# Kernel tuning notes

Hardware: AMD Instinct MI355X
Metric: run time of the kernel (lower is better)

## Reference

```python
import jax, jax.numpy as jnp
import numpy as np

HID = 512
HEADS = 8
HD = HID // HEADS
PF = 2048
EPS = 1e-5


def _layer_norm(x, g, b):
    m = jnp.mean(x, axis=-1, keepdims=True)
    v = jnp.mean((x - m) ** 2, axis=-1, keepdims=True)
    return (x - m) * jax.lax.rsqrt(v + EPS) * g + b


def setup_inputs() -> dict:
    key = jax.random.key(0)
    ks = jax.random.split(key, 24)
    s = 0.02
    p = {}
    p["src"] = jax.random.normal(ks[0], (2, 512, HID), dtype=jnp.float32)
    p["src_mask"] = jnp.ones((2, 1, 1, 512), dtype=jnp.int32)
    # projection weights stored as (in, out); Linear math y = x @ W + b
    p["Wq"] = jax.random.normal(ks[1], (HID, HID), dtype=jnp.float32) * s
    p["bq"] = jnp.zeros((HID,), jnp.float32)
    p["Wk"] = jax.random.normal(ks[2], (HID, HID), dtype=jnp.float32) * s
    p["bk"] = jnp.zeros((HID,), jnp.float32)
    p["Wv"] = jax.random.normal(ks[3], (HID, HID), dtype=jnp.float32) * s
    p["bv"] = jnp.zeros((HID,), jnp.float32)
    p["Wo"] = jax.random.normal(ks[4], (HID, HID), dtype=jnp.float32) * s
    p["bo"] = jnp.zeros((HID,), jnp.float32)
    # additive-attention params (per-head_dim)
    p["Wa"] = jax.random.normal(ks[5], (HD, HD), dtype=jnp.float32) * s
    p["ba"] = jnp.zeros((HD,), jnp.float32)
    p["Ua"] = jax.random.normal(ks[6], (HD, HD), dtype=jnp.float32) * s
    p["ub"] = jnp.zeros((HD,), jnp.float32)
    p["Vw"] = jax.random.normal(ks[7], (HD,), dtype=jnp.float32) * s
    p["Vb"] = jnp.zeros((), jnp.float32)
    # layer norms
    p["ln1_g"] = jnp.ones((HID,), jnp.float32)
    p["ln1_b"] = jnp.zeros((HID,), jnp.float32)
    p["ln2_g"] = jnp.ones((HID,), jnp.float32)
    p["ln2_b"] = jnp.zeros((HID,), jnp.float32)
    # FFN
    p["W1"] = jax.random.normal(ks[8], (HID, PF), dtype=jnp.float32) * s
    p["b1"] = jnp.zeros((PF,), jnp.float32)
    p["W2"] = jax.random.normal(ks[9], (PF, HID), dtype=jnp.float32) * s
    p["b2"] = jnp.zeros((HID,), jnp.float32)
    return p


def reference(src, src_mask, Wq, bq, Wk, bk, Wv, bv, Wo, bo,
              Wa, ba, Ua, ub, Vw, Vb, ln1_g, ln1_b, ln2_g, ln2_b,
              W1, b1, W2, b2):
    B, L, D = src.shape
    # project and split heads: (B, H, L, hd)
    def heads(x):
        return x.reshape(B, L, HEADS, HD).transpose(0, 2, 1, 3)
    Q = heads(src @ Wq + bq)
    K = heads(src @ Wk + bk)
    V = heads(src @ Wv + bv)
    Qa = Q @ Wa + ba          # (B,H,L,hd)
    Ka = K @ Ua + ub          # (B,H,L,hd)
    # additive (Bahdanau) scores: tanh broadcast to (B,H,Lq,Lk,hd), reduce with Vw
    t = jnp.tanh(Qa[:, :, :, None, :] + Ka[:, :, None, :, :])
    energy = jnp.einsum('bhqkd,d->bhqk', t, Vw) + Vb
    energy = jnp.where(src_mask == 0, jnp.float32(-1e10), energy)
    attention = jax.nn.softmax(energy, axis=-1)
    x = jnp.einsum('bhqk,bhkd->bhqd', attention, V)
    x = x.transpose(0, 2, 1, 3).reshape(B, L, D)
    attn_out = x @ Wo + bo
    src1 = _layer_norm(src + attn_out, ln1_g, ln1_b)
    ffn = jax.nn.relu(src1 @ W1 + b1) @ W2 + b2
    return _layer_norm(src1 + ffn, ln2_g, ln2_b)
```

## Files before the change

### kernel.cpp

```cpp
#include <hip/hip_runtime.h>

#define HID 512
#define HEADS 8
#define HD 64
#define PF 2048
#define LEN 512
#define EPS 1e-5f
#define LOG2E 1.44269504f

typedef __bf16 bf16x8 __attribute__((ext_vector_type(8)));
typedef float  f32x4  __attribute__((ext_vector_type(4)));

#define TC0 0.99990220f
#define TC1 (-0.33032631f)
#define TC2 0.11820859f
#define TC3 (-0.02619031f)
#define G3C1  (-0.99097893f)
#define G5C2  (0.59104295f)
#define G7C3  (-0.18333217f)
#define G10C2 (1.18208590f)
#define G21C3 (-0.54999651f)
#define G35C3 (-0.91666085f)

__device__ __forceinline__ void fuse_body(
    const float* __restrict__ Wbig, const float* __restrict__ Wsm,
    const float* __restrict__ bbig, const float* __restrict__ bsm,
    __bf16* __restrict__ outT, float* __restrict__ bout,
    int cchunk, int h, int t, float* smem) {
    float* wb_s = smem;
    float* wsm_s = smem + 4096;
    const int c0 = cchunk * 64;
    const int col = t & 63, rq = t >> 6;
    #pragma unroll
    for (int i = 0; i < 16; ++i) {
        int r = rq * 16 + i;
        wb_s[r * 64 + col]  = Wbig[(size_t)(c0 + r) * HID + h * 64 + col];
        wsm_s[r * 64 + col] = Wsm[r * 64 + col];
    }
    __syncthreads();
    float acc[16] = {};
    for (int d = 0; d < 64; ++d) {
        float wl = wsm_s[d * 64 + col];
        #pragma unroll
        for (int i = 0; i < 16; ++i)
            acc[i] += wb_s[(rq * 16 + i) * 64 + d] * wl;
    }
    #pragma unroll
    for (int i = 0; i < 16; ++i)
        outT[(size_t)(h * 64 + col) * HID + c0 + rq * 16 + i] = (__bf16)acc[i];
    if (cchunk == 0 && t < 64) {
        float bacc = bsm[col];
        for (int d = 0; d < 64; ++d)
            bacc += bbig[h * 64 + d] * wsm_s[d * 64 + col];
        bout[h * 64 + col] = bacc;
    }
}

__device__ __forceinline__ void cast_t_body(
    const float* __restrict__ W, __bf16* __restrict__ WT,
    int K, int N, int n0, int k0, int t, float* smem) {
    float* tile = smem;
    const int tx = t & 31, ty = t >> 5;
    #pragma unroll
    for (int i = 0; i < 4; ++i)
        tile[(ty + 8 * i) * 33 + tx] = W[(size_t)(k0 + ty + 8 * i) * N + n0 + tx];
    __syncthreads();
    #pragma unroll
    for (int i = 0; i < 4; ++i)
        WT[(size_t)(n0 + ty + 8 * i) * K + k0 + tx] = (__bf16)tile[tx * 33 + ty + 8 * i];
}

__global__ __launch_bounds__(256) void prep_all(
    const float* __restrict__ Wq, const float* __restrict__ Wa,
    const float* __restrict__ bq, const float* __restrict__ ba,
    const float* __restrict__ Wk, const float* __restrict__ Ua,
    const float* __restrict__ bk, const float* __restrict__ ub,
    const float* __restrict__ Wv, const float* __restrict__ bv,
    const float* __restrict__ Wo, const float* __restrict__ W1,
    const float* __restrict__ W2, const float* __restrict__ src,
    __bf16* __restrict__ WqkvT, float* __restrict__ bqkv,
    __bf16* __restrict__ WoT, __bf16* __restrict__ W1T,
    __bf16* __restrict__ W2T, __bf16* __restrict__ src_bf) {
    __shared__ float smem[8192];
    const int bid = blockIdx.x;
    const int t = threadIdx.x;
    if (bid < 64) {
        fuse_body(Wq, Wa, bq, ba, WqkvT, bqkv, bid & 7, bid >> 3, t, smem);
    } else if (bid < 128) {
        int q = bid - 64;
        fuse_body(Wk, Ua, bk, ub, WqkvT + (size_t)512 * HID, bqkv + 512, q & 7, q >> 3, t, smem);
    } else if (bid < 384) {
        int q = bid - 128;
        cast_t_body(Wv, WqkvT + (size_t)1024 * HID, HID, HID, (q & 15) * 32, (q >> 4) * 32, t, smem);
    } else if (bid < 640) {
        int q = bid - 384;
        cast_t_body(Wo, WoT, HID, HID, (q & 15) * 32, (q >> 4) * 32, t, smem);
    } else if (bid < 1664) {
        int q = bid - 640;
        cast_t_body(W1, W1T, HID, PF, (q & 63) * 32, (q >> 6) * 32, t, smem);
    } else if (bid < 2688) {
        int q = bid - 1664;
        cast_t_body(W2, W2T, PF, HID, (q & 15) * 32, (q >> 4) * 32, t, smem);
    } else if (bid < 2690) {
        int q = bid - 2688;
        bqkv[1024 + q * 256 + t] = bv[q * 256 + t];
    } else {
        int q = bid - 2690;
        int i = q * 256 + t;
        src_bf[i] = (__bf16)src[i];
    }
}

template <bool RELU, bool OUT_BF16, int KS>
__global__ __launch_bounds__(64) void gemm_mfma(
    const __bf16* __restrict__ A, const __bf16* __restrict__ BT,
    const float* __restrict__ bias, float* __restrict__ Cf,
    __bf16* __restrict__ Cb, int M, int N, int K) {
    const int m0 = blockIdx.x * 64;
    const int n0 = blockIdx.y * 64;
    const int ks = (KS > 1) ? blockIdx.z : 0;
    const int Kc = K / KS;
    const int l = threadIdx.x;
    const int r16 = l & 15;
    const int kof = (l >> 4) * 8 + ks * Kc;

    f32x4 acc[4][4] = {};
    const __bf16* Ap = A + (size_t)(m0 + r16) * K + kof;
    const __bf16* Bp = BT + (size_t)(n0 + r16) * K + kof;

    #pragma unroll 4
    for (int k0 = 0; k0 < Kc; k0 += 32) {
        bf16x8 a[4], b[4];
        #pragma unroll
        for (int mr = 0; mr < 4; ++mr)
            a[mr] = *(const bf16x8*)(Ap + (size_t)mr * 16 * K + k0);
        #pragma unroll
        for (int nr = 0; nr < 4; ++nr)
            b[nr] = *(const bf16x8*)(Bp + (size_t)nr * 16 * K + k0);
        #pragma unroll
        for (int mr = 0; mr < 4; ++mr)
            #pragma unroll
            for (int nr = 0; nr < 4; ++nr)
                acc[mr][nr] = __builtin_amdgcn_mfma_f32_16x16x32_bf16(a[mr], b[nr], acc[mr][nr], 0, 0, 0);
    }

    const int crow = (l >> 4) * 4;
    const int ccol = l & 15;
    float* Co = Cf + (size_t)ks * M * N;
    #pragma unroll
    for (int mr = 0; mr < 4; ++mr) {
        #pragma unroll
        for (int nr = 0; nr < 4; ++nr) {
            int n = n0 + nr * 16 + ccol;
            float bs = (ks == 0) ? bias[n] : 0.f;
            #pragma unroll
            for (int r = 0; r < 4; ++r) {
                int m = m0 + mr * 16 + crow + r;
                float v = acc[mr][nr][r] + bs;
                if (RELU) v = fmaxf(v, 0.f);
                if (OUT_BF16) Cb[(size_t)m * N + n] = (__bf16)v;
                else          Co[(size_t)m * N + n] = v;
            }
        }
    }
}

__global__ __launch_bounds__(64) void qkv_feat(
    const __bf16* __restrict__ A, const __bf16* __restrict__ BT,
    const float* __restrict__ bqkv, const float* __restrict__ Vw,
    __bf16* __restrict__ Af, __bf16* __restrict__ Bf,
    __bf16* __restrict__ VT) {
    __shared__ float tile[64][65];
    const int m0 = blockIdx.x * 64;
    const int by = blockIdx.y;
    const int n0 = by * 64;
    const int type = by >> 3;
    const int h = by & 7;
    const int b = m0 >> 9;
    const int bh = b * 8 + h;
    const int l0 = m0 & 511;
    const int l = threadIdx.x;
    const int r16 = l & 15;
    const int g = l >> 4;
    const int kof = g * 8;

    f32x4 acc[4][4] = {};
    const __bf16* Ap = A + (size_t)(m0 + r16) * HID + kof;
    const __bf16* Bp = BT + (size_t)(n0 + r16) * HID + kof;
    #pragma unroll 4
    for (int k0 = 0; k0 < HID; k0 += 32) {
        bf16x8 a[4], bb[4];
        #pragma unroll
        for (int mr = 0; mr < 4; ++mr)
            a[mr] = *(const bf16x8*)(Ap + (size_t)mr * 16 * HID + k0);
        #pragma unroll
        for (int nr = 0; nr < 4; ++nr)
            bb[nr] = *(const bf16x8*)(Bp + (size_t)nr * 16 * HID + k0);
        #pragma unroll
        for (int mr = 0; mr < 4; ++mr)
            #pragma unroll
            for (int nr = 0; nr < 4; ++nr)
                acc[mr][nr] = __builtin_amdgcn_mfma_f32_16x16x32_bf16(a[mr], bb[nr], acc[mr][nr], 0, 0, 0);
    }

    const int crow = g * 4;
    const int ccol = r16;
    if (type == 0) {
        #pragma unroll
        for (int nr = 0; nr < 4; ++nr) {
            int d = nr * 16 + ccol;
            float bs = bqkv[n0 + d];
            #pragma unroll
            for (int mr = 0; mr < 4; ++mr)
                #pragma unroll
                for (int r = 0; r < 4; ++r) {
                    int lrow = l0 + mr * 16 + crow + r;
                    float x = acc[mr][nr][r] + bs;
                    float x2 = x * x, x3 = x2 * x, x4 = x2 * x2, x6 = x4 * x2;
                    bf16x8 f;
                    f[0] = (__bf16)1.0f; f[1] = (__bf16)x;
                    f[2] = (__bf16)x2;   f[3] = (__bf16)x3;
                    f[4] = (__bf16)x4;   f[5] = (__bf16)(x4 * x);
                    f[6] = (__bf16)x6;   f[7] = (__bf16)(x6 * x);
                    *(bf16x8*)(Af + ((size_t)(bh * LEN + lrow)) * 512 + d * 8) = f;
                }
        }
    } else if (type == 1) {
        #pragma unroll
        for (int nr = 0; nr < 4; ++nr) {
            int d = nr * 16 + ccol;
            float bs = bqkv[n0 + d];
            float w = Vw[d];
            #pragma unroll
            for (int mr = 0; mr < 4; ++mr)
                #pragma unroll
                for (int r = 0; r < 4; ++r) {
                    int lrow = l0 + mr * 16 + crow + r;
                    float y = acc[mr][nr][r] + bs;
                    float y2 = y * y;
                    bf16x8 f;
                    f[0] = (__bf16)(w * (y * (((TC3 * y2 + TC2) * y2 + TC1) * y2 + TC0)));
                    f[1] = (__bf16)(w * (((G7C3 * y2 + G5C2) * y2 + G3C1) * y2 + TC0));
                    f[2] = (__bf16)(w * (y * ((G21C3 * y2 + G10C2) * y2 + G3C1)));
                    f[3] = (__bf16)(w * ((G35C3 * y2 + G10C2) * y2 + TC1));
                    f[4] = (__bf16)(w * (y * (G35C3 * y2 + G5C2)));
                    f[5] = (__bf16)(w * (G21C3 * y2 + TC2));
                    f[6] = (__bf16)(w * (G7C3 * y));
                    f[7] = (__bf16)(w * TC3);
                    *(bf16x8*)(Bf + ((size_t)(bh * LEN + lrow)) * 512 + d * 8) = f;
                }
        }
    } else {
        #pragma unroll
        for (int nr = 0; nr < 4; ++nr) {
            int d = nr * 16 + ccol;
            float bs = bqkv[n0 + d];
            #pragma unroll
            for (int mr = 0; mr < 4; ++mr)
                #pragma unroll
                for (int r = 0; r < 4; ++r)
                    tile[mr * 16 + crow + r][d] = acc[mr][nr][r] + bs;
        }
        __syncthreads();
        for (int dd = 0; dd < 64; ++dd)
            VT[((size_t)(bh * 64 + dd)) * LEN + l0 + l] = (__bf16)tile[l][dd];
    }
}

__global__ __launch_bounds__(256) void attn_psum(
    const __bf16* __restrict__ Af, const __bf16* __restrict__ Bf,
    const __bf16* __restrict__ VT, const int* __restrict__ mask,
    __bf16* __restrict__ X) {
    __shared__ __align__(16) char pls[32 * 1024];
    __shared__ float psum[4][16][64];
    __shared__ float rs[32][5];
    const int bid = blockIdx.x;
    const int wgid = (bid & 7) * 32 + (bid >> 3);
    const int bh = wgid >> 4;
    const int m0 = (wgid & 15) * 32;
    const int b = bh >> 3, h = bh & 7;
    const int w = threadIdx.x >> 6;
    const int l = threadIdx.x & 63;
    const int r16 = l & 15, g = l >> 4, kof = g * 8;
    const int c0 = w * 128;

    const __bf16* Ap = Af + ((size_t)(bh * LEN + m0 + r16)) * 512 + kof;
    const __bf16* Bp = Bf + ((size_t)(bh * LEN + c0 + r16)) * 512 + kof;

    f32x4 acc[2][8] = {};
    #pragma unroll 4
    for (int k0 = 0; k0 < 512; k0 += 32) {
        bf16x8 a0 = *(const bf16x8*)(Ap + k0);
        bf16x8 a1 = *(const bf16x8*)(Ap + 16 * 512 + k0);
        #pragma unroll
        for (int nr = 0; nr < 8; ++nr) {
            bf16x8 bb = *(const bf16x8*)(Bp + (size_t)nr * 16 * 512 + k0);
            acc[0][nr] = __builtin_amdgcn_mfma_f32_16x16x32_bf16(a0, bb, acc[0][nr], 0, 0, 0);
            acc[1][nr] = __builtin_amdgcn_mfma_f32_16x16x32_bf16(a1, bb, acc[1][nr], 0, 0, 0);
        }
    }

    float rsum[2][4] = {};
    #pragma unroll
    for (int nr = 0; nr < 8; ++nr) {
        int col = c0 + nr * 16 + r16;
        float mk = (mask[b * LEN + col] == 0) ? 0.f : 1.f;
        #pragma unroll
        for (int mr = 0; mr < 2; ++mr)
            #pragma unroll
            for (int r = 0; r < 4; ++r) {
                float pv = __builtin_amdgcn_exp2f(acc[mr][nr][r] * LOG2E) * mk;
                acc[mr][nr][r] = pv;
                rsum[mr][r] += pv;
            }
    }
    #pragma unroll
    for (int off = 1; off <= 8; off <<= 1)
        #pragma unroll
        for (int mr = 0; mr < 2; ++mr)
            #pragma unroll
            for (int r = 0; r < 4; ++r)
                rsum[mr][r] += __shfl_xor(rsum[mr][r], off);
    if (r16 == 0) {
        #pragma unroll
        for (int mr = 0; mr < 2; ++mr)
            #pragma unroll
            for (int r = 0; r < 4; ++r)
                rs[mr * 16 + g * 4 + r][w] = rsum[mr][r];
    }
    __syncthreads();
    float inv_[2][4];
    #pragma unroll
    for (int mr = 0; mr < 2; ++mr)
        #pragma unroll
        for (int r = 0; r < 4; ++r) {
            int row = mr * 16 + g * 4 + r;
            float tot = rs[row][0] + rs[row][1] + rs[row][2] + rs[row][3];
            inv_[mr][r] = __builtin_amdgcn_rcpf(tot);
        }
    #pragma unroll
    for (int mr = 0; mr < 2; ++mr)
        #pragma unroll
        for (int nr = 0; nr < 8; ++nr) {
            int col = c0 + nr * 16 + r16;
            #pragma unroll
            for (int r = 0; r < 4; ++r) {
                int row = mr * 16 + g * 4 + r;
                int byte = (row * 1024 + col * 2) ^ ((row & 7) << 4);
                *(__bf16*)(pls + byte) = (__bf16)(acc[mr][nr][r] * inv_[mr][r]);
            }
        }
    __syncthreads();

    const int rh = w >> 1, kh = w & 1;
    f32x4 oc[4] = {};
    const __bf16* Vp = VT + ((size_t)(bh * 64 + r16)) * LEN + kh * 256 + kof;
    #pragma unroll 4
    for (int k0 = 0; k0 < 256; k0 += 32) {
        int row = rh * 16 + r16;
        int byte = (row * 1024 + (kh * 256 + k0 + kof) * 2) ^ ((row & 7) << 4);
        bf16x8 pa = *(const bf16x8*)(pls + byte);
        #pragma unroll
        for (int nr = 0; nr < 4; ++nr) {
            bf16x8 vb = *(const bf16x8*)(Vp + (size_t)nr * 16 * LEN + k0);
            oc[nr] = __builtin_amdgcn_mfma_f32_16x16x32_bf16(pa, vb, oc[nr], 0, 0, 0);
        }
    }
    #pragma unroll
    for (int nr = 0; nr < 4; ++nr)
        #pragma unroll
        for (int r = 0; r < 4; ++r)
            psum[w][g * 4 + r][nr * 16 + r16] = oc[nr][r];
    __syncthreads();
    for (int i = threadIdx.x; i < 32 * 64; i += 256) {
        int row = i >> 6, d = i & 63;
        int rh2 = row >> 4, rr = row & 15;
        float v = psum[rh2 * 2][rr][d] + psum[rh2 * 2 + 1][rr][d];
        X[(size_t)(b * LEN + m0 + row) * HID + h * 64 + d] = (__bf16)v;
    }
}

template <bool WB, int NS>
__global__ __launch_bounds__(256) void ln_kernel(
    const float* __restrict__ A, const float* __restrict__ Bsrc,
    const float* __restrict__ g, const float* __restrict__ beta,
    float* __restrict__ out, __bf16* __restrict__ outb) {
    const int row = blockIdx.x;
    const int t = threadIdx.x;
    float x0 = Bsrc[(size_t)row * HID + t];
    float x1 = Bsrc[(size_t)row * HID + t + 256];
    #pragma unroll
    for (int s = 0; s < NS; ++s) {
        x0 += A[(size_t)s * 524288 + (size_t)row * HID + t];
        x1 += A[(size_t)s * 524288 + (size_t)row * HID + t + 256];
    }
    float s0 = x0 + x1, ss = x0 * x0 + x1 * x1;
    #pragma unroll
    for (int off = 32; off; off >>= 1) {
        s0 += __shfl_xor(s0, off);
        ss += __shfl_xor(ss, off);
    }
    __shared__ float rsm[4], rss[4];
    const int lane = t & 63, wv = t >> 6;
    if (lane == 0) { rsm[wv] = s0; rss[wv] = ss; }
    __syncthreads();
    s0 = rsm[0] + rsm[1] + rsm[2] + rsm[3];
    ss = rss[0] + rss[1] + rss[2] + rss[3];
    float mean = s0 * (1.0f / HID);
    float var = ss * (1.0f / HID) - mean * mean;
    float inv = rsqrtf(var + EPS);
    float y0 = (x0 - mean) * inv * g[t] + beta[t];
    float y1 = (x1 - mean) * inv * g[t + 256] + beta[t + 256];
    out[(size_t)row * HID + t] = y0;
    out[(size_t)row * HID + t + 256] = y1;
    if (WB) {
        outb[(size_t)row * HID + t] = (__bf16)y0;
        outb[(size_t)row * HID + t + 256] = (__bf16)y1;
    }
}


extern "C" void kernel_launch(void* const* d_in, const int* in_sizes, int n_in,
                              void* d_out, int out_size, void* d_ws, size_t ws_size,
                              hipStream_t stream) {
    const float* src   = (const float*)d_in[0];
    const int*   mask  = (const int*)d_in[1];
    const float* Wq    = (const float*)d_in[2];
    const float* bq    = (const float*)d_in[3];
    const float* Wk    = (const float*)d_in[4];
    const float* bk    = (const float*)d_in[5];
    const float* Wv    = (const float*)d_in[6];
    const float* bv    = (const float*)d_in[7];
    const float* Wo    = (const float*)d_in[8];
    const float* bo    = (const float*)d_in[9];
    const float* Wa    = (const float*)d_in[10];
    const float* ba    = (const float*)d_in[11];
    const float* Ua    = (const float*)d_in[12];
    const float* ub    = (const float*)d_in[13];
    const float* Vw    = (const float*)d_in[14];
    const float* ln1g  = (const float*)d_in[16];
    const float* ln1b  = (const float*)d_in[17];
    const float* ln2g  = (const float*)d_in[18];
    const float* ln2b  = (const float*)d_in[19];
    const float* W1    = (const float*)d_in[20];
    const float* b1    = (const float*)d_in[21];
    const float* W2    = (const float*)d_in[22];
    const float* b2    = (const float*)d_in[23];
    float* out = (float*)d_out;

    float* ws = (float*)d_ws;
    size_t off = 0;
    auto alloc = [&](size_t nf) { float* p = ws + off; off += nf; return p; };

    __bf16* WqkvT  = (__bf16*)alloc(393216);
    __bf16* WoT    = (__bf16*)alloc(131072);
    __bf16* W1T    = (__bf16*)alloc(524288);
    __bf16* W2T    = (__bf16*)alloc(524288);
    float*  bqkv   = alloc(1536);
    __bf16* src_bf = (__bf16*)alloc(262144);
    __bf16* Af     = (__bf16*)alloc(2097152);
    __bf16* Bf     = (__bf16*)alloc(2097152);
    __bf16* VT     = (__bf16*)alloc(262144);
    __bf16* x_bf   = (__bf16*)alloc(262144);
    float*  tmp    = alloc(2097152);
    float*  src1   = alloc(524288);
    __bf16* s1_bf  = (__bf16*)alloc(262144);
    __bf16* h1     = (__bf16*)alloc(1048576);

    const int M = 2 * LEN;

    prep_all<<<4738, 256, 0, stream>>>(Wq, Wa, bq, ba, Wk, Ua, bk, ub,
                                       Wv, bv, Wo, W1, W2, src,
                                       WqkvT, bqkv, WoT, W1T, W2T, src_bf);

    qkv_feat<<<dim3(16, 24), 64, 0, stream>>>(src_bf, WqkvT, bqkv, Vw, Af, Bf, VT);

    attn_psum<<<256, 256, 0, stream>>>(Af, Bf, VT, mask, x_bf);

    gemm_mfma<false, false, 2><<<dim3(16, 8, 2), 64, 0, stream>>>(
        x_bf, WoT, bo, tmp, nullptr, M, HID, HID);

    ln_kernel<true, 2><<<M, 256, 0, stream>>>(tmp, src, ln1g, ln1b, src1, s1_bf);

    gemm_mfma<true, true, 1><<<dim3(16, 32), 64, 0, stream>>>(
        s1_bf, W1T, b1, nullptr, h1, M, PF, HID);

    gemm_mfma<false, false, 4><<<dim3(16, 8, 4), 64, 0, stream>>>(
        h1, W2T, b2, tmp, nullptr, M, HID, PF);

    ln_kernel<false, 4><<<M, 256, 0, stream>>>(tmp, src1, ln2g, ln2b, out, nullptr);
}
```

Baseline: 102.2 us.

## Fuse all stages into one cooperative persistent kernel with grid syncs

Replaces the eight separate kernel launches with a single cooperative kernel of 256 blocks. Grid-wide barriers separate the stages, and each stage distributes its work units over blocks or waves. The goal is to remove launch gaps and per-kernel ramp-up between the short stages. The V transpose becomes its own stage through a raw buffer, and layer norm is rewritten to handle one row per wave with vector loads. The costs are grid.sync overhead, lower occupancy from a large shared-memory footprint, and fixed parallelism of 256 blocks.

New measurement: 385.1 us. +276.9%, slower.

```diff
diff --git a/kernel.cpp b/kernel.cpp
--- a/kernel.cpp
+++ b/kernel.cpp
@@ -1,4 +1,7 @@
 #include <hip/hip_runtime.h>
+#include <hip/hip_cooperative_groups.h>
+
+namespace cg = cooperative_groups;
 
 #define HID 512
 #define HEADS 8
@@ -22,6 +25,19 @@
 #define G21C3 (-0.54999651f)
 #define G35C3 (-0.91666085f)
 
+struct MegaArgs {
+    const float* src; const int* mask;
+    const float *Wq, *bq, *Wk, *bk, *Wv, *bv, *Wo, *bo;
+    const float *Wa, *ba, *Ua, *ub, *Vw;
+    const float *ln1g, *ln1b, *ln2g, *ln2b;
+    const float *W1, *b1, *W2, *b2;
+    float* out;
+    __bf16* WqkvT; float* bqkv;
+    __bf16 *WoT, *W1T, *W2T, *src_bf, *Af, *Bf, *vraw, *VT, *x_bf;
+    float *tmp, *src1;
+    __bf16 *s1_bf, *h1;
+};
+
 __device__ __forceinline__ void fuse_body(
     const float* __restrict__ Wbig, const float* __restrict__ Wsm,
     const float* __restrict__ bbig, const float* __restrict__ bsm,
@@ -70,57 +86,15 @@
         WT[(size_t)(n0 + ty + 8 * i) * K + k0 + tx] = (__bf16)tile[tx * 33 + ty + 8 * i];
 }
 
-__global__ __launch_bounds__(256) void prep_all(
-    const float* __restrict__ Wq, const float* __restrict__ Wa,
-    const float* __restrict__ bq, const float* __restrict__ ba,
-    const float* __restrict__ Wk, const float* __restrict__ Ua,
-    const float* __restrict__ bk, const float* __restrict__ ub,
-    const float* __restrict__ Wv, const float* __restrict__ bv,
-    const float* __restrict__ Wo, const float* __restrict__ W1,
-    const float* __restrict__ W2, const float* __restrict__ src,
-    __bf16* __restrict__ WqkvT, float* __restrict__ bqkv,
-    __bf16* __restrict__ WoT, __bf16* __restrict__ W1T,
-    __bf16* __restrict__ W2T, __bf16* __restrict__ src_bf) {
-    __shared__ float smem[8192];
-    const int bid = blockIdx.x;
-    const int t = threadIdx.x;
-    if (bid < 64) {
-        fuse_body(Wq, Wa, bq, ba, WqkvT, bqkv, bid & 7, bid >> 3, t, smem);
-    } else if (bid < 128) {
-        int q = bid - 64;
-        fuse_body(Wk, Ua, bk, ub, WqkvT + (size_t)512 * HID, bqkv + 512, q & 7, q >> 3, t, smem);
-    } else if (bid < 384) {
-        int q = bid - 128;
-        cast_t_body(Wv, WqkvT + (size_t)1024 * HID, HID, HID, (q & 15) * 32, (q >> 4) * 32, t, smem);
-    } else if (bid < 640) {
-        int q = bid - 384;
-        cast_t_body(Wo, WoT, HID, HID, (q & 15) * 32, (q >> 4) * 32, t, smem);
-    } else if (bid < 1664) {
-        int q = bid - 640;
-        cast_t_body(W1, W1T, HID, PF, (q & 63) * 32, (q >> 6) * 32, t, smem);
-    } else if (bid < 2688) {
-        int q = bid - 1664;
-        cast_t_body(W2, W2T, PF, HID, (q & 15) * 32, (q >> 4) * 32, t, smem);
-    } else if (bid < 2690) {
-        int q = bid - 2688;
-        bqkv[1024 + q * 256 + t] = bv[q * 256 + t];
-    } else {
-        int q = bid - 2690;
-        int i = q * 256 + t;
-        src_bf[i] = (__bf16)src[i];
-    }
-}
-
 template <bool RELU, bool OUT_BF16, int KS>
-__global__ __launch_bounds__(64) void gemm_mfma(
+__device__ __forceinline__ void gemm_wave(
     const __bf16* __restrict__ A, const __bf16* __restrict__ BT,
     const float* __restrict__ bias, float* __restrict__ Cf,
-    __bf16* __restrict__ Cb, int M, int N, int K) {
-    const int m0 = blockIdx.x * 64;
-    const int n0 = blockIdx.y * 64;
-    const int ks = (KS > 1) ? blockIdx.z : 0;
+    __bf16* __restrict__ Cb, int M, int N, int K,
+    int bx, int by, int ks, int l) {
+    const int m0 = bx * 64;
+    const int n0 = by * 64;
     const int Kc = K / KS;
-    const int l = threadIdx.x;
     const int r16 = l & 15;
     const int kof = (l >> 4) * 8 + ks * Kc;
 
@@ -165,34 +139,28 @@
     }
 }
 
-__global__ __launch_bounds__(64) void qkv_feat(
-    const __bf16* __restrict__ A, const __bf16* __restrict__ BT,
-    const float* __restrict__ bqkv, const float* __restrict__ Vw,
-    __bf16* __restrict__ Af, __bf16* __restrict__ Bf,
-    __bf16* __restrict__ VT) {
-    __shared__ float tile[64][65];
-    const int m0 = blockIdx.x * 64;
-    const int by = blockIdx.y;
+__device__ __forceinline__ void qkv_wave(const MegaArgs& a, int u, int l) {
+    const int bx = u & 15, by = u >> 4;
+    const int m0 = bx * 64;
     const int n0 = by * 64;
     const int type = by >> 3;
     const int h = by & 7;
     const int b = m0 >> 9;
     const int bh = b * 8 + h;
     const int l0 = m0 & 511;
-    const int l = threadIdx.x;
     const int r16 = l & 15;
     const int g = l >> 4;
     const int kof = g * 8;
 
     f32x4 acc[4][4] = {};
-    const __bf16* Ap = A + (size_t)(m0 + r16) * HID + kof;
-    const __bf16* Bp = BT + (size_t)(n0 + r16) * HID + kof;
+    const __bf16* Ap = a.src_bf + (size_t)(m0 + r16) * HID + kof;
+    const __bf16* Bp = a.WqkvT + (size_t)(n0 + r16) * HID + kof;
     #pragma unroll 4
     for (int k0 = 0; k0 < HID; k0 += 32) {
-        bf16x8 a[4], bb[4];
+        bf16x8 av[4], bb[4];
         #pragma unroll
         for (int mr = 0; mr < 4; ++mr)
-            a[mr] = *(const bf16x8*)(Ap + (size_t)mr * 16 * HID + k0);
+            av[mr] = *(const bf16x8*)(Ap + (size_t)mr * 16 * HID + k0);
         #pragma unroll
         for (int nr = 0; nr < 4; ++nr)
             bb[nr] = *(const bf16x8*)(Bp + (size_t)nr * 16 * HID + k0);
@@ -200,16 +168,15 @@
         for (int mr = 0; mr < 4; ++mr)
             #pragma unroll
             for (int nr = 0; nr < 4; ++nr)
-                acc[mr][nr] = __builtin_amdgcn_mfma_f32_16x16x32_bf16(a[mr], bb[nr], acc[mr][nr], 0, 0, 0);
+                acc[mr][nr] = __builtin_amdgcn_mfma_f32_16x16x32_bf16(av[mr], bb[nr], acc[mr][nr], 0, 0, 0);
     }
 
     const int crow = g * 4;
-    const int ccol = r16;
     if (type == 0) {
         #pragma unroll
         for (int nr = 0; nr < 4; ++nr) {
-            int d = nr * 16 + ccol;
-            float bs = bqkv[n0 + d];
+            int d = nr * 16 + r16;
+            float bs = a.bqkv[n0 + d];
             #pragma unroll
             for (int mr = 0; mr < 4; ++mr)
                 #pragma unroll
@@ -222,15 +189,15 @@
                     f[2] = (__bf16)x2;   f[3] = (__bf16)x3;
                     f[4] = (__bf16)x4;   f[5] = (__bf16)(x4 * x);
                     f[6] = (__bf16)x6;   f[7] = (__bf16)(x6 * x);
-                    *(bf16x8*)(Af + ((size_t)(bh * LEN + lrow)) * 512 + d * 8) = f;
+                    *(bf16x8*)(a.Af + ((size_t)(bh * LEN + lrow)) * 512 + d * 8) = f;
                 }
         }
     } else if (type == 1) {
         #pragma unroll
         for (int nr = 0; nr < 4; ++nr) {
-            int d = nr * 16 + ccol;
-            float bs = bqkv[n0 + d];
-            float w = Vw[d];
+            int d = nr * 16 + r16;
+            float bs = a.bqkv[n0 + d];
+            float w = a.Vw[d];
             #pragma unroll
             for (int mr = 0; mr < 4; ++mr)
                 #pragma unroll
@@ -247,246 +214,309 @@
                     f[5] = (__bf16)(w * (G21C3 * y2 + TC2));
                     f[6] = (__bf16)(w * (G7C3 * y));
                     f[7] = (__bf16)(w * TC3);
-                    *(bf16x8*)(Bf + ((size_t)(bh * LEN + lrow)) * 512 + d * 8) = f;
+                    *(bf16x8*)(a.Bf + ((size_t)(bh * LEN + lrow)) * 512 + d * 8) = f;
                 }
         }
     } else {
         #pragma unroll
         for (int nr = 0; nr < 4; ++nr) {
-            int d = nr * 16 + ccol;
-            float bs = bqkv[n0 + d];
+            int d = nr * 16 + r16;
+            float bs = a.bqkv[1024 + h * 64 + d];
             #pragma unroll
             for (int mr = 0; mr < 4; ++mr)
                 #pragma unroll
-                for (int r = 0; r < 4; ++r)
-                    tile[mr * 16 + crow + r][d] = acc[mr][nr][r] + bs;
-        }
-        __syncthreads();
-        for (int dd = 0; dd < 64; ++dd)
-            VT[((size_t)(bh * 64 + dd)) * LEN + l0 + l] = (__bf16)tile[l][dd];
-    }
-}
-
-__global__ __launch_bounds__(256) void attn_psum(
-    const __bf16* __restrict__ Af, const __bf16* __restrict__ Bf,
-    const __bf16* __restrict__ VT, const int* __restrict__ mask,
-    __bf16* __restrict__ X) {
-    __shared__ __align__(16) char pls[32 * 1024];
-    __shared__ float psum[4][16][64];
-    __shared__ float rs[32][5];
-    const int bid = blockIdx.x;
-    const int wgid = (bid & 7) * 32 + (bid >> 3);
-    const int bh = wgid >> 4;
-    const int m0 = (wgid & 15) * 32;
-    const int b = bh >> 3, h = bh & 7;
-    const int w = threadIdx.x >> 6;
-    const int l = threadIdx.x & 63;
-    const int r16 = l & 15, g = l >> 4, kof = g * 8;
-    const int c0 = w * 128;
-
-    const __bf16* Ap = Af + ((size_t)(bh * LEN + m0 + r16)) * 512 + kof;
-    const __bf16* Bp = Bf + ((size_t)(bh * LEN + c0 + r16)) * 512 + kof;
-
-    f32x4 acc[2][8] = {};
-    #pragma unroll 4
-    for (int k0 = 0; k0 < 512; k0 += 32) {
-        bf16x8 a0 = *(const bf16x8*)(Ap + k0);
-        bf16x8 a1 = *(const bf16x8*)(Ap + 16 * 512 + k0);
-        #pragma unroll
-        for (int nr = 0; nr < 8; ++nr) {
-            bf16x8 bb = *(const bf16x8*)(Bp + (size_t)nr * 16 * 512 + k0);
-            acc[0][nr] = __builtin_amdgcn_mfma_f32_16x16x32_bf16(a0, bb, acc[0][nr], 0, 0, 0);
-            acc[1][nr] = __builtin_amdgcn_mfma_f32_16x16x32_bf16(a1, bb, acc[1][nr], 0, 0, 0);
-        }
-    }
-
-    float rsum[2][4] = {};
-    #pragma unroll
-    for (int nr = 0; nr < 8; ++nr) {
-        int col = c0 + nr * 16 + r16;
-        float mk = (mask[b * LEN + col] == 0) ? 0.f : 1.f;
-        #pragma unroll
-        for (int mr = 0; mr < 2; ++mr)
-            #pragma unroll
-            for (int r = 0; r < 4; ++r) {
-                float pv = __builtin_amdgcn_exp2f(acc[mr][nr][r] * LOG2E) * mk;
-                acc[mr][nr][r] = pv;
-                rsum[mr][r] += pv;
-            }
-    }
-    #pragma unroll
-    for (int off = 1; off <= 8; off <<= 1)
-        #pragma unroll
-        for (int mr = 0; mr < 2; ++mr)
-            #pragma unroll
-            for (int r = 0; r < 4; ++r)
-                rsum[mr][r] += __shfl_xor(rsum[mr][r], off);
-    if (r16 == 0) {
-        #pragma unroll
-        for (int mr = 0; mr < 2; ++mr)
-            #pragma unroll
-            for (int r = 0; r < 4; ++r)
-                rs[mr * 16 + g * 4 + r][w] = rsum[mr][r];
-    }
-    __syncthreads();
-    float inv_[2][4];
-    #pragma unroll
-    for (int mr = 0; mr < 2; ++mr)
-        #pragma unroll
-        for (int r = 0; r < 4; ++r) {
-            int row = mr * 16 + g * 4 + r;
-            float tot = rs[row][0] + rs[row][1] + rs[row][2] + rs[row][3];
-            inv_[mr][r] = __builtin_amdgcn_rcpf(tot);
-        }
-    #pragma unroll
-    for (int mr = 0; mr < 2; ++mr)
-        #pragma unroll
-        for (int nr = 0; nr < 8; ++nr) {
-            int col = c0 + nr * 16 + r16;
-            #pragma unroll
-            for (int r = 0; r < 4; ++r) {
-                int row = mr * 16 + g * 4 + r;
-                int byte = (row * 1024 + col * 2) ^ ((row & 7) << 4);
-                *(__bf16*)(pls + byte) = (__bf16)(acc[mr][nr][r] * inv_[mr][r]);
-            }
-        }
-    __syncthreads();
-
-    const int rh = w >> 1, kh = w & 1;
-    f32x4 oc[4] = {};
-    const __bf16* Vp = VT + ((size_t)(bh * 64 + r16)) * LEN + kh * 256 + kof;
-    #pragma unroll 4
-    for (int k0 = 0; k0 < 256; k0 += 32) {
-        int row = rh * 16 + r16;
-        int byte = (row * 1024 + (kh * 256 + k0 + kof) * 2) ^ ((row & 7) << 4);
-        bf16x8 pa = *(const bf16x8*)(pls + byte);
-        #pragma unroll
-        for (int nr = 0; nr < 4; ++nr) {
-            bf16x8 vb = *(const bf16x8*)(Vp + (size_t)nr * 16 * LEN + k0);
-            oc[nr] = __builtin_amdgcn_mfma_f32_16x16x32_bf16(pa, vb, oc[nr], 0, 0, 0);
-        }
-    }
-    #pragma unroll
-    for (int nr = 0; nr < 4; ++nr)
-        #pragma unroll
-        for (int r = 0; r < 4; ++r)
-            psum[w][g * 4 + r][nr * 16 + r16] = oc[nr][r];
-    __syncthreads();
-    for (int i = threadIdx.x; i < 32 * 64; i += 256) {
-        int row = i >> 6, d = i & 63;
-        int rh2 = row >> 4, rr = row & 15;
-        float v = psum[rh2 * 2][rr][d] + psum[rh2 * 2 + 1][rr][d];
-        X[(size_t)(b * LEN + m0 + row) * HID + h * 64 + d] = (__bf16)v;
+                for (int r = 0; r < 4; ++r) {
+                    int m = m0 + mr * 16 + crow + r;
+                    a.vraw[(size_t)m * 512 + h * 64 + d] = (__bf16)(acc[mr][nr][r] + bs);
+                }
+        }
     }
 }
 
 template <bool WB, int NS>
-__global__ __launch_bounds__(256) void ln_kernel(
+__device__ __forceinline__ void ln_row(
     const float* __restrict__ A, const float* __restrict__ Bsrc,
     const float* __restrict__ g, const float* __restrict__ beta,
-    float* __restrict__ out, __bf16* __restrict__ outb) {
-    const int row = blockIdx.x;
-    const int t = threadIdx.x;
-    float x0 = Bsrc[(size_t)row * HID + t];
-    float x1 = Bsrc[(size_t)row * HID + t + 256];
+    float* __restrict__ out, __bf16* __restrict__ outb, int row, int lane) {
+    const int c = lane * 8;
+    f32x4 v0 = *(const f32x4*)(Bsrc + (size_t)row * HID + c);
+    f32x4 v1 = *(const f32x4*)(Bsrc + (size_t)row * HID + c + 4);
     #pragma unroll
     for (int s = 0; s < NS; ++s) {
-        x0 += A[(size_t)s * 524288 + (size_t)row * HID + t];
-        x1 += A[(size_t)s * 524288 + (size_t)row * HID + t + 256];
-    }
-    float s0 = x0 + x1, ss = x0 * x0 + x1 * x1;
+        v0 += *(const f32x4*)(A + (size_t)s * 524288 + (size_t)row * HID + c);
+        v1 += *(const f32x4*)(A + (size_t)s * 524288 + (size_t)row * HID + c + 4);
+    }
+    float s0 = 0.f, ss = 0.f;
+    #pragma unroll
+    for (int j = 0; j < 4; ++j) { s0 += v0[j] + v1[j]; ss += v0[j] * v0[j] + v1[j] * v1[j]; }
     #pragma unroll
     for (int off = 32; off; off >>= 1) {
         s0 += __shfl_xor(s0, off);
         ss += __shfl_xor(ss, off);
     }
-    __shared__ float rsm[4], rss[4];
-    const int lane = t & 63, wv = t >> 6;
-    if (lane == 0) { rsm[wv] = s0; rss[wv] = ss; }
-    __syncthreads();
-    s0 = rsm[0] + rsm[1] + rsm[2] + rsm[3];
-    ss = rss[0] + rss[1] + rss[2] + rss[3];
     float mean = s0 * (1.0f / HID);
     float var = ss * (1.0f / HID) - mean * mean;
     float inv = rsqrtf(var + EPS);
-    float y0 = (x0 - mean) * inv * g[t] + beta[t];
-    float y1 = (x1 - mean) * inv * g[t + 256] + beta[t + 256];
-    out[(size_t)row * HID + t] = y0;
-    out[(size_t)row * HID + t + 256] = y1;
+    f32x4 g0 = *(const f32x4*)(g + c), g1 = *(const f32x4*)(g + c + 4);
+    f32x4 b0 = *(const f32x4*)(beta + c), b1 = *(const f32x4*)(beta + c + 4);
+    f32x4 y0, y1;
+    #pragma unroll
+    for (int j = 0; j < 4; ++j) {
+        y0[j] = (v0[j] - mean) * inv * g0[j] + b0[j];
+        y1[j] = (v1[j] - mean) * inv * g1[j] + b1[j];
+    }
+    *(f32x4*)(out + (size_t)row * HID + c) = y0;
+    *(f32x4*)(out + (size_t)row * HID + c + 4) = y1;
     if (WB) {
-        outb[(size_t)row * HID + t] = (__bf16)y0;
-        outb[(size_t)row * HID + t + 256] = (__bf16)y1;
-    }
+        bf16x8 yb;
+        #pragma unroll
+        for (int j = 0; j < 4; ++j) { yb[j] = (__bf16)y0[j]; yb[4 + j] = (__bf16)y1[j]; }
+        *(bf16x8*)(outb + (size_t)row * HID + c) = yb;
+    }
+}
+
+__global__ __launch_bounds__(256, 2) void mega(MegaArgs a) {
+    __shared__ __align__(16) char lds[49792];
+    cg::grid_group grid = cg::this_grid();
+    const int t = threadIdx.x;
+    const int nb = gridDim.x;
+    const int nw = nb * 4;
+    const int wid = blockIdx.x * 4 + (t >> 6);
+    const int l = t & 63;
+
+    for (int u = blockIdx.x; u < 4738; u += nb) {
+        float* smem = (float*)lds;
+        if (u < 64) {
+            fuse_body(a.Wq, a.Wa, a.bq, a.ba, a.WqkvT, a.bqkv, u & 7, u >> 3, t, smem);
+        } else if (u < 128) {
+            int q = u - 64;
+            fuse_body(a.Wk, a.Ua, a.bk, a.ub, a.WqkvT + (size_t)512 * HID, a.bqkv + 512, q & 7, q >> 3, t, smem);
+        } else if (u < 384) {
+            int q = u - 128;
+            cast_t_body(a.Wv, a.WqkvT + (size_t)1024 * HID, HID, HID, (q & 15) * 32, (q >> 4) * 32, t, smem);
+        } else if (u < 640) {
+            int q = u - 384;
+            cast_t_body(a.Wo, a.WoT, HID, HID, (q & 15) * 32, (q >> 4) * 32, t, smem);
+        } else if (u < 1664) {
+            int q = u - 640;
+            cast_t_body(a.W1, a.W1T, HID, PF, (q & 63) * 32, (q >> 6) * 32, t, smem);
+        } else if (u < 2688) {
+            int q = u - 1664;
+            cast_t_body(a.W2, a.W2T, PF, HID, (q & 15) * 32, (q >> 4) * 32, t, smem);
+        } else if (u < 2690) {
+            int q = u - 2688;
+            a.bqkv[1024 + q * 256 + t] = a.bv[q * 256 + t];
+        } else {
+            int q = u - 2690;
+            int i = q * 256 + t;
+            a.src_bf[i] = (__bf16)a.src[i];
+        }
+        __syncthreads();
+    }
+    grid.sync();
+
+    for (int u = wid; u < 384; u += nw) qkv_wave(a, u, l);
+    grid.sync();
+
+    for (int u = blockIdx.x; u < 128; u += nb) {
+        float* tile = (float*)lds;
+        const int bh = u >> 3, b = bh >> 3, h = bh & 7;
+        const int k0 = (u & 7) * 64;
+        const int tx = t & 63, ty = t >> 6;
+        #pragma unroll
+        for (int i = 0; i < 16; ++i) {
+            int r = ty + 4 * i;
+            tile[r * 65 + tx] = (float)a.vraw[(size_t)(b * LEN + k0 + r) * 512 + h * 64 + tx];
+        }
+        __syncthreads();
+        #pragma unroll
+        for (int i = 0; i < 16; ++i) {
+            int dd = ty + 4 * i;
+            a.VT[((size_t)(bh * 64 + dd)) * LEN + k0 + tx] = (__bf16)tile[tx * 65 + dd];
+        }
+        __syncthreads();
+    }
+    grid.sync();
+
+    for (int u = blockIdx.x; u < 256; u += nb) {
+        char* pls = lds;
+        float* psum = (float*)(lds + 32768);
+        float* rs = (float*)(lds + 32768 + 16384);
+        const int wgid = (u & 7) * 32 + (u >> 3);
+        const int bh = wgid >> 4;
+        const int m0 = (wgid & 15) * 32;
+        const int b = bh >> 3, h = bh & 7;
+        const int w = t >> 6;
+        const int r16 = l & 15, g = l >> 4, kof = g * 8;
+        const int c0 = w * 128;
+
+        const __bf16* Ap = a.Af + ((size_t)(bh * LEN + m0 + r16)) * 512 + kof;
+        const __bf16* Bp = a.Bf + ((size_t)(bh * LEN + c0 + r16)) * 512 + kof;
+
+        f32x4 acc[2][8] = {};
+        #pragma unroll 4
+        for (int k0 = 0; k0 < 512; k0 += 32) {
+            bf16x8 a0 = *(const bf16x8*)(Ap + k0);
+            bf16x8 a1 = *(const bf16x8*)(Ap + 16 * 512 + k0);
+            #pragma unroll
+            for (int nr = 0; nr < 8; ++nr) {
+                bf16x8 bb = *(const bf16x8*)(Bp + (size_t)nr * 16 * 512 + k0);
+                acc[0][nr] = __builtin_amdgcn_mfma_f32_16x16x32_bf16(a0, bb, acc[0][nr], 0, 0, 0);
+                acc[1][nr] = __builtin_amdgcn_mfma_f32_16x16x32_bf16(a1, bb, acc[1][nr], 0, 0, 0);
+            }
+        }
+
+        float rsum[2][4] = {};
+        #pragma unroll
+        for (int nr = 0; nr < 8; ++nr) {
+            int col = c0 + nr * 16 + r16;
+            float mk = (a.mask[b * LEN + col] == 0) ? 0.f : 1.f;
+            #pragma unroll
+            for (int mr = 0; mr < 2; ++mr)
+                #pragma unroll
+                for (int r = 0; r < 4; ++r) {
+                    float pv = __builtin_amdgcn_exp2f(acc[mr][nr][r] * LOG2E) * mk;
+                    acc[mr][nr][r] = pv;
+                    rsum[mr][r] += pv;
+                }
+        }
+        #pragma unroll
+        for (int off = 1; off <= 8; off <<= 1)
+            #pragma unroll
+            for (int mr = 0; mr < 2; ++mr)
+                #pragma unroll
+                for (int r = 0; r < 4; ++r)
+                    rsum[mr][r] += __shfl_xor(rsum[mr][r], off);
+        if (r16 == 0) {
+            #pragma unroll
+            for (int mr = 0; mr < 2; ++mr)
+                #pragma unroll
+                for (int r = 0; r < 4; ++r)
+                    rs[(mr * 16 + g * 4 + r) * 5 + w] = rsum[mr][r];
+        }
+        __syncthreads();
+        float inv_[2][4];
+        #pragma unroll
+        for (int mr = 0; mr < 2; ++mr)
+            #pragma unroll
+            for (int r = 0; r < 4; ++r) {
+                int row = mr * 16 + g * 4 + r;
+                float tot = rs[row * 5 + 0] + rs[row * 5 + 1] + rs[row * 5 + 2] + rs[row * 5 + 3];
+                inv_[mr][r] = __builtin_amdgcn_rcpf(tot);
+            }
+        #pragma unroll
+        for (int mr = 0; mr < 2; ++mr)
+            #pragma unroll
+            for (int nr = 0; nr < 8; ++nr) {
+                int col = c0 + nr * 16 + r16;
+                #pragma unroll
+                for (int r = 0; r < 4; ++r) {
+                    int row = mr * 16 + g * 4 + r;
+                    int byte = (row * 1024 + col * 2) ^ ((row & 7) << 4);
+                    *(__bf16*)(pls + byte) = (__bf16)(acc[mr][nr][r] * inv_[mr][r]);
+                }
+            }
+        __syncthreads();
+
+        const int rh = w >> 1, kh = w & 1;
+        f32x4 oc[4] = {};
+        const __bf16* Vp = a.VT + ((size_t)(bh * 64 + r16)) * LEN + kh * 256 + kof;
+        #pragma unroll 4
+        for (int k0 = 0; k0 < 256; k0 += 32) {
+            int row = rh * 16 + r16;
+            int byte = (row * 1024 + (kh * 256 + k0 + kof) * 2) ^ ((row & 7) << 4);
+            bf16x8 pa = *(const bf16x8*)(pls + byte);
+            #pragma unroll
+            for (int nr = 0; nr < 4; ++nr) {
+                bf16x8 vb = *(const bf16x8*)(Vp + (size_t)nr * 16 * LEN + k0);
+                oc[nr] = __builtin_amdgcn_mfma_f32_16x16x32_bf16(pa, vb, oc[nr], 0, 0, 0);
+            }
+        }
+        #pragma unroll
+        for (int nr = 0; nr < 4; ++nr)
+            #pragma unroll
+            for (int r = 0; r < 4; ++r)
+                psum[(w * 16 + g * 4 + r) * 64 + nr * 16 + r16] = oc[nr][r];
+        __syncthreads();
+        for (int i = t; i < 32 * 64; i += 256) {
+            int row = i >> 6, d = i & 63;
+            int rh2 = row >> 4, rr = row & 15;
+            float v = psum[(rh2 * 2 * 16 + rr) * 64 + d] + psum[((rh2 * 2 + 1) * 16 + rr) * 64 + d];
+            a.x_bf[(size_t)(b * LEN + m0 + row) * HID + h * 64 + d] = (__bf16)v;
+        }
+        __syncthreads();
+    }
+    grid.sync();
+
+    for (int u = wid; u < 256; u += nw) {
+        int bx = u & 15, by = (u >> 4) & 7, ks = u >> 7;
+        gemm_wave<false, false, 2>(a.x_bf, a.WoT, a.bo, a.tmp, nullptr,
+                                   1024, HID, HID, bx, by, ks, l);
+    }
+    grid.sync();
+
+    for (int u = wid; u < 1024; u += nw)
+        ln_row<true, 2>(a.tmp, a.src, a.ln1g, a.ln1b, a.src1, a.s1_bf, u, l);
+    grid.sync();
+
+    for (int u = wid; u < 512; u += nw) {
+        int bx = u & 15, by = u >> 4;
+        gemm_wave<true, true, 1>(a.s1_bf, a.W1T, a.b1, nullptr, a.h1,
+                                 1024, PF, HID, bx, by, 0, l);
+    }
+    grid.sync();
+
+    for (int u = wid; u < 512; u += nw) {
+        int bx = u & 15, by = (u >> 4) & 7, ks = u >> 7;
+        gemm_wave<false, false, 4>(a.h1, a.W2T, a.b2, a.tmp, nullptr,
+                                   1024, HID, PF, bx, by, ks, l);
+    }
+    grid.sync();
+
+    for (int u = wid; u < 1024; u += nw)
+        ln_row<false, 4>(a.tmp, a.src1, a.ln2g, a.ln2b, a.out, nullptr, u, l);
 }
 
 
 extern "C" void kernel_launch(void* const* d_in, const int* in_sizes, int n_in,
                               void* d_out, int out_size, void* d_ws, size_t ws_size,
                               hipStream_t stream) {
-    const float* src   = (const float*)d_in[0];
-    const int*   mask  = (const int*)d_in[1];
-    const float* Wq    = (const float*)d_in[2];
-    const float* bq    = (const float*)d_in[3];
-    const float* Wk    = (const float*)d_in[4];
-    const float* bk    = (const float*)d_in[5];
-    const float* Wv    = (const float*)d_in[6];
-    const float* bv    = (const float*)d_in[7];
-    const float* Wo    = (const float*)d_in[8];
-    const float* bo    = (const float*)d_in[9];
-    const float* Wa    = (const float*)d_in[10];
-    const float* ba    = (const float*)d_in[11];
-    const float* Ua    = (const float*)d_in[12];
-    const float* ub    = (const float*)d_in[13];
-    const float* Vw    = (const float*)d_in[14];
-    const float* ln1g  = (const float*)d_in[16];
-    const float* ln1b  = (const float*)d_in[17];
-    const float* ln2g  = (const float*)d_in[18];
-    const float* ln2b  = (const float*)d_in[19];
-    const float* W1    = (const float*)d_in[20];
-    const float* b1    = (const float*)d_in[21];
-    const float* W2    = (const float*)d_in[22];
-    const float* b2    = (const float*)d_in[23];
-    float* out = (float*)d_out;
+    MegaArgs a;
+    a.src  = (const float*)d_in[0];
+    a.mask = (const int*)d_in[1];
+    a.Wq = (const float*)d_in[2];  a.bq = (const float*)d_in[3];
+    a.Wk = (const float*)d_in[4];  a.bk = (const float*)d_in[5];
+    a.Wv = (const float*)d_in[6];  a.bv = (const float*)d_in[7];
+    a.Wo = (const float*)d_in[8];  a.bo = (const float*)d_in[9];
+    a.Wa = (const float*)d_in[10]; a.ba = (const float*)d_in[11];
+    a.Ua = (const float*)d_in[12]; a.ub = (const float*)d_in[13];
+    a.Vw = (const float*)d_in[14];
+    a.ln1g = (const float*)d_in[16]; a.ln1b = (const float*)d_in[17];
+    a.ln2g = (const float*)d_in[18]; a.ln2b = (const float*)d_in[19];
+    a.W1 = (const float*)d_in[20]; a.b1 = (const float*)d_in[21];
+    a.W2 = (const float*)d_in[22]; a.b2 = (const float*)d_in[23];
+    a.out = (float*)d_out;
 
     float* ws = (float*)d_ws;
     size_t off = 0;
     auto alloc = [&](size_t nf) { float* p = ws + off; off += nf; return p; };
 
-    __bf16* WqkvT  = (__bf16*)alloc(393216);
-    __bf16* WoT    = (__bf16*)alloc(131072);
-    __bf16* W1T    = (__bf16*)alloc(524288);
-    __bf16* W2T    = (__bf16*)alloc(524288);
-    float*  bqkv   = alloc(1536);
-    __bf16* src_bf = (__bf16*)alloc(262144);
-    __bf16* Af     = (__bf16*)alloc(2097152);
-    __bf16* Bf     = (__bf16*)alloc(2097152);
-    __bf16* VT     = (__bf16*)alloc(262144);
-    __bf16* x_bf   = (__bf16*)alloc(262144);
-    float*  tmp    = alloc(2097152);
-    float*  src1   = alloc(524288);
-    __bf16* s1_bf  = (__bf16*)alloc(262144);
-    __bf16* h1     = (__bf16*)alloc(1048576);
-
-    const int M = 2 * LEN;
-
-    prep_all<<<4738, 256, 0, stream>>>(Wq, Wa, bq, ba, Wk, Ua, bk, ub,
-                                       Wv, bv, Wo, W1, W2, src,
-                                       WqkvT, bqkv, WoT, W1T, W2T, src_bf);
-
-    qkv_feat<<<dim3(16, 24), 64, 0, stream>>>(src_bf, WqkvT, bqkv, Vw, Af, Bf, VT);
-
-    attn_psum<<<256, 256, 0, stream>>>(Af, Bf, VT, mask, x_bf);
-
-    gemm_mfma<false, false, 2><<<dim3(16, 8, 2), 64, 0, stream>>>(
-        x_bf, WoT, bo, tmp, nullptr, M, HID, HID);
-
-    ln_kernel<true, 2><<<M, 256, 0, stream>>>(tmp, src, ln1g, ln1b, src1, s1_bf);
-
-    gemm_mfma<true, true, 1><<<dim3(16, 32), 64, 0, stream>>>(
-        s1_bf, W1T, b1, nullptr, h1, M, PF, HID);
-
-    gemm_mfma<false, false, 4><<<dim3(16, 8, 4), 64, 0, stream>>>(
-        h1, W2T, b2, tmp, nullptr, M, HID, PF);
-
-    ln_kernel<false, 4><<<M, 256, 0, stream>>>(tmp, src1, ln2g, ln2b, out, nullptr);
-}
+    a.WqkvT  = (__bf16*)alloc(393216);
+    a.WoT    = (__bf16*)alloc(131072);
+    a.W1T    = (__bf16*)alloc(524288);
+    a.W2T    = (__bf16*)alloc(524288);
+    a.bqkv   = alloc(1536);
+    a.src_bf = (__bf16*)alloc(262144);
+    a.Af     = (__bf16*)alloc(2097152);
+    a.Bf     = (__bf16*)alloc(2097152);
+    a.vraw   = (__bf16*)alloc(262144);
+    a.VT     = (__bf16*)alloc(262144);
+    a.x_bf   = (__bf16*)alloc(262144);
+    a.tmp    = alloc(2097152);
+    a.src1   = alloc(524288);
+    a.s1_bf  = (__bf16*)alloc(262144);
+    a.h1     = (__bf16*)alloc(1048576);
+
+    void* kp[] = { &a };
+    hipLaunchCooperativeKernel((void*)mega, dim3(256), dim3(256), kp, 0, stream);
+}
```
